# Kernel optimization log

Hardware: AMD Instinct MI355X
Metric: run time of the kernel (lower is better)

The kernel has to match this reference:

```python
import jax, jax.numpy as jnp
import numpy as np

DIM_MODEL = 1024
HEADS = 16
DIM_PER_HEAD = DIM_MODEL // HEADS


def setup_inputs() -> dict:
    key = jax.random.key(0)
    k0, k1, k2, k3, k4 = jax.random.split(key, 5)
    x = jax.random.normal(k0, (2, 2048, DIM_MODEL), dtype=jnp.float32)
    # combined_linear: dim_model -> 3*dim_model (torch Linear: y = x @ W.T + b)
    s_in = 1.0 / np.sqrt(DIM_MODEL)
    W_qkv = jax.random.uniform(k1, (3 * DIM_MODEL, DIM_MODEL), minval=-s_in, maxval=s_in, dtype=jnp.float32)
    b_qkv = jax.random.uniform(k2, (3 * DIM_MODEL,), minval=-s_in, maxval=s_in, dtype=jnp.float32)
    W_out = jax.random.uniform(k3, (DIM_MODEL, DIM_MODEL), minval=-s_in, maxval=s_in, dtype=jnp.float32)
    b_out = jax.random.uniform(k4, (DIM_MODEL,), minval=-s_in, maxval=s_in, dtype=jnp.float32)
    return {"x": x, "W_qkv": W_qkv, "b_qkv": b_qkv, "W_out": W_out, "b_out": b_out}


def reference(x, W_qkv, b_qkv, W_out, b_out):
    B, S, D = x.shape
    H, Dh = HEADS, DIM_PER_HEAD
    qkv = x @ W_qkv.T + b_qkv  # [B, S, 3D]
    q, k, v = jnp.split(qkv, 3, axis=2)
    # [B, H, S, Dh]
    q = q.reshape(B, S, H, Dh).transpose(0, 2, 1, 3)
    k = k.reshape(B, S, H, Dh).transpose(0, 2, 1, 3)
    v = v.reshape(B, S, H, Dh).transpose(0, 2, 1, 3)
    scores = jnp.einsum('bhqd,bhkd->bhqk', q, k) / jnp.sqrt(jnp.float32(Dh))
    causal = jnp.tril(jnp.ones((S, S), dtype=bool))
    scores = jnp.where(causal[None, None, :, :], scores, -jnp.inf)
    p_attn = jax.nn.softmax(scores, axis=-1)
    out = jnp.einsum('bhqk,bhkd->bhqd', p_attn, v)
    out = out.transpose(0, 2, 1, 3).reshape(B, S, D)
    return out @ W_out.T + b_out
```

## Files before the change

kernel.cpp:

```cpp
#include <hip/hip_runtime.h>
#include <cstdint>

typedef __attribute__((ext_vector_type(8))) __bf16 bf16x8;
typedef __attribute__((ext_vector_type(4))) float f32x4;
typedef __attribute__((ext_vector_type(8))) short short8;
typedef __attribute__((ext_vector_type(4))) float float4v;
typedef __attribute__((ext_vector_type(4))) unsigned uint4v;
typedef __attribute__((ext_vector_type(4))) unsigned short ushort4v;

__device__ __forceinline__ unsigned short f2bf(float f) {
    unsigned u = __builtin_bit_cast(unsigned, f);
    u += 0x7fffu + ((u >> 16) & 1u);
    return (unsigned short)(u >> 16);
}
__device__ __forceinline__ float bf2f(unsigned short s) {
    return __builtin_bit_cast(float, (unsigned)s << 16);
}
__device__ __forceinline__ f32x4 mfma_bf16(bf16x8 a, bf16x8 b, f32x4 c) {
    return __builtin_amdgcn_mfma_f32_16x16x32_bf16(a, b, c, 0, 0, 0);
}
__device__ __forceinline__ unsigned pkbf(float lo, float hi) {
    unsigned r;
    asm("v_cvt_pk_bf16_f32 %0, %1, %2" : "=v"(r) : "v"(lo), "v"(hi));
    return r;
}

#define GLD16(g, l)                                                                     \
    __builtin_amdgcn_global_load_lds((const __attribute__((address_space(1))) void*)(g), \
                                     (__attribute__((address_space(3))) void*)(l), 16, 0, 0)

__global__ void __launch_bounds__(256) cvt_all(const float* __restrict__ x,
                                               const float* __restrict__ wqkv,
                                               const float* __restrict__ wout,
                                               unsigned short* __restrict__ xb,
                                               unsigned short* __restrict__ wqb,
                                               unsigned short* __restrict__ wob) {
    int i = blockIdx.x * blockDim.x + threadIdx.x;
#pragma unroll
    for (int k = 0; k < 2; k++, i += 524288) {
        const float* s;
        unsigned short* d;
        int off;
        if (i < 524288)      { s = x;    d = xb;  off = i; }
        else if (i < 917504) { s = wqkv; d = wqb; off = i - 524288; }
        else                 { s = wout; d = wob; off = i - 917504; }
        const float4v* sp = (const float4v*)(s + (size_t)off * 8);
        float4v v0 = sp[0], v1 = sp[1];
        uint4v u;
        u[0] = pkbf(v0[0], v0[1]);
        u[1] = pkbf(v0[2], v0[3]);
        u[2] = pkbf(v1[0], v1[1]);
        u[3] = pkbf(v1[2], v1[3]);
        *(uint4v*)(d + (size_t)off * 8) = u;
    }
}

template <int MODE>
__global__ void __launch_bounds__(256) gemm_bt(const unsigned short* __restrict__ A,
                                               const unsigned short* __restrict__ B,
                                               const float* __restrict__ bias,
                                               void* __restrict__ C,
                                               unsigned short* __restrict__ vT,
                                               int M, int N, int K) {
    __shared__ __attribute__((aligned(16))) unsigned short As[2][128 * 32];
    __shared__ __attribute__((aligned(16))) unsigned short Bs[2][128 * 32];
    const int tid = threadIdx.x;
    const int w = tid >> 6, lane = tid & 63;
    const int a = lane & 15, g = lane >> 4;

    const int cpx = gridDim.x >> 3;
    const int nf = ((int)blockIdx.x & 7) * cpx + ((int)blockIdx.x >> 3);
    const int bx = nf >> 5;
    const int by = nf & 31;
    const int m0 = by * 128, n0 = bx * 128;
    const int wr = (w >> 1) * 64, wc = (w & 1) * 64;

    f32x4 acc[4][4];
#pragma unroll
    for (int i = 0; i < 4; i++)
#pragma unroll
        for (int j = 0; j < 4; j++) acc[i][j] = (f32x4)(0.0f);

    const int r0 = tid >> 2;
    const int c0 = (tid & 3) * 8;
    const unsigned short* gA0 = A + (size_t)(m0 + r0) * K + c0;
    const unsigned short* gA1 = A + (size_t)(m0 + 64 + r0) * K + c0;
    const unsigned short* gB0 = B + (size_t)(n0 + r0) * K + c0;
    const unsigned short* gB1 = B + (size_t)(n0 + 64 + r0) * K + c0;

#define GSTAGE(buf_, k0_)                                               \
    {                                                                   \
        char* la_ = (char*)&As[buf_][0] + w * 1024;                     \
        char* lb_ = (char*)&Bs[buf_][0] + w * 1024;                     \
        GLD16(gA0 + (k0_), la_);                                        \
        GLD16(gA1 + (k0_), la_ + 4096);                                 \
        GLD16(gB0 + (k0_), lb_);                                        \
        GLD16(gB1 + (k0_), lb_ + 4096);                                 \
    }

    GSTAGE(0, 0);
    __syncthreads();

    int cur = 0;
    for (int k0 = 0; k0 < K; k0 += 32) {
        if (k0 + 32 < K) GSTAGE(cur ^ 1, k0 + 32);

        bf16x8 af[4], bfr[4];
#pragma unroll
        for (int i = 0; i < 4; i++) {
            af[i]  = *(const bf16x8*)&As[cur][(wr + i * 16 + a) * 32 + g * 8];
            bfr[i] = *(const bf16x8*)&Bs[cur][(wc + i * 16 + a) * 32 + g * 8];
        }
#pragma unroll
        for (int i = 0; i < 4; i++)
#pragma unroll
            for (int j = 0; j < 4; j++) acc[i][j] = mfma_bf16(af[i], bfr[j], acc[i][j]);

        __syncthreads();
        cur ^= 1;
    }
#undef GSTAGE

#pragma unroll
    for (int j = 0; j < 4; j++) {
        const int col = n0 + wc + j * 16 + a;
        const float bv = bias[col];
        if (MODE == 0) {
            float* Cf = (float*)C;
#pragma unroll
            for (int i = 0; i < 4; i++)
#pragma unroll
                for (int jr = 0; jr < 4; jr++) {
                    const int row = m0 + wr + i * 16 + g * 4 + jr;
                    Cf[(size_t)row * N + col] = acc[i][j][jr] + bv;
                }
        } else if (n0 < 2048) {
            unsigned short* Cb = (unsigned short*)C;
#pragma unroll
            for (int i = 0; i < 4; i++)
#pragma unroll
                for (int jr = 0; jr < 4; jr++) {
                    const int row = m0 + wr + i * 16 + g * 4 + jr;
                    Cb[(size_t)row * 2048 + col] = f2bf(acc[i][j][jr] + bv);
                }
        } else {
            const int vd = col - 2048;
            const int hh = vd >> 6, dd = vd & 63;
#pragma unroll
            for (int i = 0; i < 4; i++) {
                const int token0 = m0 + wr + i * 16 + g * 4;
                const int bb = token0 >> 11, kl = token0 & 2047;
                ushort4v st;
#pragma unroll
                for (int jr = 0; jr < 4; jr++) st[jr] = f2bf(acc[i][j][jr] + bv);
                *(ushort4v*)(vT + ((size_t)((bb << 4) + hh) * 64 + dd) * 2048 + kl) = st;
            }
        }
    }
}


#define STAGE(bf_, t_)                                                  \
    {                                                                   \
        const size_t ko_ = (size_t)(t_) * 128 * LDQ;                    \
        const size_t vo_ = (size_t)(t_) * 128;                          \
        char* db_ = (char*)&KV[bf_][0] + w * 1024;                      \
        GLD16(sK0 + ko_, db_);                                          \
        GLD16(sK1 + ko_, db_ + 8192);                                   \
        GLD16(sV0 + vo_, db_ + 16384);                                  \
        GLD16(sV1 + vo_, db_ + 24576);                                  \
    }

__global__ void __launch_bounds__(512, 4) attn_fwd(const unsigned short* __restrict__ qk,
                                                   const unsigned short* __restrict__ vT,
                                                   unsigned short* __restrict__ o) {
    constexpr int SL = 2048, DH = 64, LDQ = 2048;
    constexpr float GAMMA = 0.18033688011112042f;
    const int bh = blockIdx.x & 31;
    const int s = blockIdx.x >> 5;
    const int qb = (s < 8) ? 15 - s : s - 8;
    const int b = bh >> 4, h = bh & 15;
    const int tid = threadIdx.x;
    const int w = tid >> 6, lane = tid & 63;
    const int n = lane & 15, g = lane >> 4;

    __shared__ __attribute__((aligned(16))) unsigned short KV[2][16384];

    const int qs = qb * 128 + w * 16 + n;
    const int nt = qb + 1;

    bf16x8 qf[2];
    {
        const unsigned short* qp = qk + (size_t)(b * SL + qs) * LDQ + h * DH + g * 8;
        short8 la = *(const short8*)qp, lb = *(const short8*)(qp + 32);
        short8 s0, s1;
#pragma unroll
        for (int e = 0; e < 8; e++) {
            s0[e] = (short)f2bf(bf2f((unsigned short)la[e]) * GAMMA);
            s1[e] = (short)f2bf(bf2f((unsigned short)lb[e]) * GAMMA);
        }
        qf[0] = __builtin_bit_cast(bf16x8, s0);
        qf[1] = __builtin_bit_cast(bf16x8, s1);
    }

    const int rK = tid >> 3;
    const int xrK = (rK & 3) | (((rK >> 3) & 1) << 2);
    const int csK = (((tid & 7) ^ xrK) << 3);
    const unsigned short* sK0 = qk + (size_t)(b * SL + rK) * LDQ + 1024 + h * DH + csK;
    const unsigned short* sK1 = sK0 + (size_t)64 * LDQ;
    const int dV = tid >> 4;
    const int csV = (((tid & 15) ^ (dV & 7)) << 3);
    const unsigned short* sV0 = vT + (size_t)bh * DH * SL + (size_t)dV * SL + csV;
    const unsigned short* sV1 = sV0 + (size_t)32 * SL;

    const int srow = 8 * (n >> 2) + (n & 3);
    const int xrq = (n & 3) | (((n >> 2) & 1) << 2);
    const int offK0 = ((g ^ xrq) << 3);
    const int offK1 = offK0 ^ 32;
    int offV[4];
#pragma unroll
    for (int kc = 0; kc < 4; kc++) offV[kc] = (((4 * kc + g) ^ (n & 7)) << 3);

    f32x4 of[4];
#pragma unroll
    for (int i = 0; i < 4; i++) of[i] = (f32x4)(0.0f);
    float m_i = -1e30f, l_i = 0.0f;

    STAGE(0, 0);
    __syncthreads();

    for (int t = 0; t < nt; ++t) {
        const unsigned short* kvb = &KV[t & 1][0];
        if (t + 1 < nt) STAGE((t & 1) ^ 1, t + 1);

        f32x4 p[8];
        __builtin_amdgcn_s_setprio(1);
#pragma unroll
        for (int f = 0; f < 8; f++) {
            const int r_ = srow + ((f >> 1) << 5) + ((f & 1) << 2);
            const bf16x8 ka_ = *(const bf16x8*)&kvb[r_ * 64 + offK0];
            const bf16x8 kc_ = *(const bf16x8*)&kvb[r_ * 64 + offK1];
            f32x4 acc_ = (f32x4)(0.0f);
            acc_ = mfma_bf16(ka_, qf[0], acc_);
            acc_ = mfma_bf16(kc_, qf[1], acc_);
            p[f] = acc_;
        }
        __builtin_amdgcn_s_setprio(0);

        if (t == nt - 1) {
            const int k0 = t * 128;
#pragma unroll
            for (int f = 0; f < 8; f++) {
                const int kb_ = k0 + ((f >> 1) << 5) + ((f & 1) << 2) + 8 * g;
#pragma unroll
                for (int e = 0; e < 4; e++)
                    if (kb_ + e > qs) p[f][e] = -1e30f;
            }
        }

        float mx = -1e30f;
#pragma unroll
        for (int f = 0; f < 8; f++) {
            const float a_ = fmaxf(fmaxf(p[f][0], p[f][1]), fmaxf(p[f][2], p[f][3]));
            mx = fmaxf(mx, a_);
        }
        mx = fmaxf(mx, __shfl_xor(mx, 16));
        mx = fmaxf(mx, __shfl_xor(mx, 32));
        if (!__all(mx <= m_i + 8.0f)) {
            const float mn_ = fmaxf(m_i, mx);
            const float al_ = __builtin_amdgcn_exp2f(m_i - mn_);
            l_i *= al_;
#pragma unroll
            for (int d_ = 0; d_ < 4; d_++) of[d_] = of[d_] * al_;
            m_i = mn_;
        }
        float rs = 0.0f;
#pragma unroll
        for (int f = 0; f < 8; f++)
#pragma unroll
            for (int e = 0; e < 4; e++) {
                p[f][e] = __builtin_amdgcn_exp2f(p[f][e] - m_i);
                rs += p[f][e];
            }
        l_i += rs;

        bf16x8 pf[4];
#pragma unroll
        for (int kc = 0; kc < 4; kc++) {
            uint4v u_;
            u_[0] = pkbf(p[2 * kc][0], p[2 * kc][1]);
            u_[1] = pkbf(p[2 * kc][2], p[2 * kc][3]);
            u_[2] = pkbf(p[2 * kc + 1][0], p[2 * kc + 1][1]);
            u_[3] = pkbf(p[2 * kc + 1][2], p[2 * kc + 1][3]);
            pf[kc] = __builtin_bit_cast(bf16x8, u_);
        }

        const unsigned short* vb = kvb + 8192;
        __builtin_amdgcn_s_setprio(1);
#pragma unroll
        for (int df = 0; df < 4; df++) {
            const int vrow = (df * 16 + n) * 128;
#pragma unroll
            for (int kc = 0; kc < 4; kc++) {
                const bf16x8 va_ = *(const bf16x8*)&vb[vrow + offV[kc]];
                of[df] = mfma_bf16(va_, pf[kc], of[df]);
            }
        }
        __builtin_amdgcn_s_setprio(0);

        __syncthreads();
    }

    float rl = l_i;
    rl += __shfl_xor(rl, 16);
    rl += __shfl_xor(rl, 32);
    const float inv = 1.0f / rl;
    unsigned short* op = o + (size_t)(b * SL + qs) * 1024 + h * DH + 4 * g;
#pragma unroll
    for (int df = 0; df < 4; df++) {
        ushort4v st;
#pragma unroll
        for (int r = 0; r < 4; r++) st[r] = f2bf(of[df][r] * inv);
        *(ushort4v*)(op + df * 16) = st;
    }
}

extern "C" void kernel_launch(void* const* d_in, const int* in_sizes, int n_in,
                              void* d_out, int out_size, void* d_ws, size_t ws_size,
                              hipStream_t stream) {
    (void)in_sizes; (void)n_in; (void)out_size; (void)ws_size;
    const float* x    = (const float*)d_in[0];
    const float* Wqkv = (const float*)d_in[1];
    const float* bqkv = (const float*)d_in[2];
    const float* Wout = (const float*)d_in[3];
    const float* bout = (const float*)d_in[4];
    float* out = (float*)d_out;

    const int BS = 2, SL = 2048, DM = 1024;
    const int M = BS * SL;
    const int N1 = 3 * DM;
    const int K = DM;

    char* ws = (char*)d_ws;
    unsigned short* x_bf    = (unsigned short*)(ws);
    unsigned short* wqkv_bf = (unsigned short*)(ws + (8u << 20));
    unsigned short* wout_bf = (unsigned short*)(ws + (14u << 20));
    unsigned short* qkbuf   = (unsigned short*)(ws + (16u << 20));
    unsigned short* vTbuf   = (unsigned short*)(ws + (32u << 20));
    unsigned short* attn_o  = (unsigned short*)(ws + (40u << 20));

    cvt_all<<<2048, 256, 0, stream>>>(x, Wqkv, Wout, x_bf, wqkv_bf, wout_bf);

    gemm_bt<1><<<dim3(N1 / 128 * (M / 128)), 256, 0, stream>>>(x_bf, wqkv_bf, bqkv, qkbuf, vTbuf, M, N1, K);

    attn_fwd<<<dim3(512), 512, 0, stream>>>(qkbuf, vTbuf, attn_o);

    gemm_bt<0><<<dim3(DM / 128 * (M / 128)), 256, 0, stream>>>(attn_o, wout_bf, bout, out, nullptr, M, DM, K);
}
```

Baseline: 105.1 us.

## Add dedicated 256x192-tile QKV GEMM with swizzled LDS and interleaved staging

```diff
diff --git a/kernel.cpp b/kernel.cpp
--- a/kernel.cpp
+++ b/kernel.cpp
@@ -55,12 +55,126 @@
     }
 }
 
-template <int MODE>
+
+#define STG_A(bf_, i_, t_) \
+    GLD16(gA + (size_t)(i_) * 64 * 1024 + (size_t)(t_) * 64, (char*)&Asl[bf_][0] + (i_) * 8192 + w * 1024)
+#define STG_B(bf_, i_, t_) \
+    GLD16(gB + (size_t)(i_) * 64 * 1024 + (size_t)(t_) * 64, (char*)&Bsl[bf_][0] + (i_) * 8192 + w * 1024)
+
+#define LDA(c_, mf_, kk_) \
+    (*(const bf16x8*)((const char*)&Asl[c_][0] + (wm * 128 + (mf_) * 16 + a) * 128 + (((((kk_) << 2) + g) ^ xa) << 4)))
+#define LDB(c_, nf_, kk_) \
+    (*(const bf16x8*)((const char*)&Bsl[c_][0] + (wn * 48 + (nf_) * 16 + a) * 128 + (((((kk_) << 2) + g) ^ xa) << 4)))
+
+#define PHASE(c_, mb_)                                                        \
+    {                                                                         \
+        bf16x8 a0_ = LDA(c_, mb_, 0), a1_ = LDA(c_, mb_, 1);                  \
+        bf16x8 a2_ = LDA(c_, (mb_) + 1, 0), a3_ = LDA(c_, (mb_) + 1, 1);      \
+        __builtin_amdgcn_s_setprio(1);                                        \
+        _Pragma("unroll") for (int nf_ = 0; nf_ < 3; nf_++) {                 \
+            acc[mb_][nf_]       = mfma_bf16(a0_, bfr[nf_][0], acc[mb_][nf_]);       \
+            acc[mb_][nf_]       = mfma_bf16(a1_, bfr[nf_][1], acc[mb_][nf_]);       \
+            acc[(mb_) + 1][nf_] = mfma_bf16(a2_, bfr[nf_][0], acc[(mb_) + 1][nf_]); \
+            acc[(mb_) + 1][nf_] = mfma_bf16(a3_, bfr[nf_][1], acc[(mb_) + 1][nf_]); \
+        }                                                                     \
+        __builtin_amdgcn_s_setprio(0);                                        \
+    }
+
+__global__ void __launch_bounds__(512, 2) gemm_qkv(const unsigned short* __restrict__ A,
+                                                   const unsigned short* __restrict__ B,
+                                                   const float* __restrict__ bias,
+                                                   unsigned short* __restrict__ qkbuf,
+                                                   unsigned short* __restrict__ vT) {
+    constexpr int K = 1024;
+    __shared__ __attribute__((aligned(16))) unsigned short Asl[2][256 * 64];
+    __shared__ __attribute__((aligned(16))) unsigned short Bsl[2][192 * 64];
+    const int tid = threadIdx.x;
+    const int w = tid >> 6, lane = tid & 63;
+    const int a = lane & 15, g = lane >> 4;
+    const int xa = a & 7;
+    const int wm = w >> 2, wn = w & 3;
+
+    const int nfb = ((int)blockIdx.x & 7) * 32 + ((int)blockIdx.x >> 3);
+    const int bx = nfb >> 4, by = nfb & 15;
+    const int m0 = by * 256, n0 = bx * 192;
+
+    f32x4 acc[8][3];
+#pragma unroll
+    for (int i = 0; i < 8; i++)
+#pragma unroll
+        for (int j = 0; j < 3; j++) acc[i][j] = (f32x4)(0.0f);
+
+    const int rA = tid >> 3, uA = tid & 7;
+    const unsigned short* gA = A + (size_t)(m0 + rA) * K + ((uA ^ (rA & 7)) << 3);
+    const unsigned short* gB = B + (size_t)(n0 + rA) * K + ((uA ^ (rA & 7)) << 3);
+
+    STG_A(0, 0, 0); STG_A(0, 1, 0); STG_A(0, 2, 0); STG_A(0, 3, 0);
+    STG_B(0, 0, 0); STG_B(0, 1, 0); STG_B(0, 2, 0);
+
+    for (int t = 0; t < 16; ++t) {
+        const int c = t & 1, nx = c ^ 1;
+        const bool more = (t < 15);
+
+        if (more) { STG_A(nx, 0, t + 1); STG_A(nx, 1, t + 1); }
+        if (more) asm volatile("s_waitcnt vmcnt(2)" ::: "memory");
+        else      asm volatile("s_waitcnt vmcnt(0)" ::: "memory");
+        __builtin_amdgcn_s_barrier();
+
+        bf16x8 bfr[3][2];
+#pragma unroll
+        for (int nf = 0; nf < 3; nf++) {
+            bfr[nf][0] = LDB(c, nf, 0);
+            bfr[nf][1] = LDB(c, nf, 1);
+        }
+        PHASE(c, 0);
+        __builtin_amdgcn_s_barrier();
+
+        if (more) { STG_A(nx, 2, t + 1); STG_A(nx, 3, t + 1); }
+        PHASE(c, 2);
+        __builtin_amdgcn_s_barrier();
+
+        if (more) { STG_B(nx, 0, t + 1); STG_B(nx, 1, t + 1); }
+        PHASE(c, 4);
+        __builtin_amdgcn_s_barrier();
+
+        if (more) { STG_B(nx, 2, t + 1); }
+        PHASE(c, 6);
+        asm volatile("" ::: "memory");
+        __builtin_amdgcn_s_barrier();
+    }
+
+#pragma unroll
+    for (int nf = 0; nf < 3; nf++) {
+        const int cb = n0 + wn * 48 + nf * 16;
+        const int col = cb + a;
+        const float bv = bias[col];
+        if (cb < 2048) {
+#pragma unroll
+            for (int mf = 0; mf < 8; mf++)
+#pragma unroll
+                for (int jr = 0; jr < 4; jr++) {
+                    const int row = m0 + wm * 128 + mf * 16 + g * 4 + jr;
+                    qkbuf[(size_t)row * 2048 + col] = f2bf(acc[mf][nf][jr] + bv);
+                }
+        } else {
+            const int vd = col - 2048, hh = vd >> 6, dd = vd & 63;
+#pragma unroll
+            for (int mf = 0; mf < 8; mf++) {
+                const int t0 = m0 + wm * 128 + mf * 16 + g * 4;
+                const int bb = t0 >> 11, kl = t0 & 2047;
+                ushort4v st;
+#pragma unroll
+                for (int jr = 0; jr < 4; jr++) st[jr] = f2bf(acc[mf][nf][jr] + bv);
+                *(ushort4v*)(vT + ((size_t)((bb << 4) + hh) * 64 + dd) * 2048 + kl) = st;
+            }
+        }
+    }
+}
+
 __global__ void __launch_bounds__(256) gemm_bt(const unsigned short* __restrict__ A,
                                                const unsigned short* __restrict__ B,
                                                const float* __restrict__ bias,
-                                               void* __restrict__ C,
-                                               unsigned short* __restrict__ vT,
+                                               float* __restrict__ C,
                                                int M, int N, int K) {
     __shared__ __attribute__((aligned(16))) unsigned short As[2][128 * 32];
     __shared__ __attribute__((aligned(16))) unsigned short Bs[2][128 * 32];
@@ -125,37 +239,13 @@
     for (int j = 0; j < 4; j++) {
         const int col = n0 + wc + j * 16 + a;
         const float bv = bias[col];
-        if (MODE == 0) {
-            float* Cf = (float*)C;
-#pragma unroll
-            for (int i = 0; i < 4; i++)
-#pragma unroll
-                for (int jr = 0; jr < 4; jr++) {
-                    const int row = m0 + wr + i * 16 + g * 4 + jr;
-                    Cf[(size_t)row * N + col] = acc[i][j][jr] + bv;
-                }
-        } else if (n0 < 2048) {
-            unsigned short* Cb = (unsigned short*)C;
-#pragma unroll
-            for (int i = 0; i < 4; i++)
-#pragma unroll
-                for (int jr = 0; jr < 4; jr++) {
-                    const int row = m0 + wr + i * 16 + g * 4 + jr;
-                    Cb[(size_t)row * 2048 + col] = f2bf(acc[i][j][jr] + bv);
-                }
-        } else {
-            const int vd = col - 2048;
-            const int hh = vd >> 6, dd = vd & 63;
-#pragma unroll
-            for (int i = 0; i < 4; i++) {
-                const int token0 = m0 + wr + i * 16 + g * 4;
-                const int bb = token0 >> 11, kl = token0 & 2047;
-                ushort4v st;
-#pragma unroll
-                for (int jr = 0; jr < 4; jr++) st[jr] = f2bf(acc[i][j][jr] + bv);
-                *(ushort4v*)(vT + ((size_t)((bb << 4) + hh) * 64 + dd) * 2048 + kl) = st;
+#pragma unroll
+        for (int i = 0; i < 4; i++)
+#pragma unroll
+            for (int jr = 0; jr < 4; jr++) {
+                const int row = m0 + wr + i * 16 + g * 4 + jr;
+                C[(size_t)row * N + col] = acc[i][j][jr] + bv;
             }
-        }
     }
 }
 
@@ -338,7 +428,6 @@
 
     const int BS = 2, SL = 2048, DM = 1024;
     const int M = BS * SL;
-    const int N1 = 3 * DM;
     const int K = DM;
 
     char* ws = (char*)d_ws;
@@ -351,9 +440,9 @@
 
     cvt_all<<<2048, 256, 0, stream>>>(x, Wqkv, Wout, x_bf, wqkv_bf, wout_bf);
 
-    gemm_bt<1><<<dim3(N1 / 128 * (M / 128)), 256, 0, stream>>>(x_bf, wqkv_bf, bqkv, qkbuf, vTbuf, M, N1, K);
+    gemm_qkv<<<dim3(256), 512, 0, stream>>>(x_bf, wqkv_bf, bqkv, qkbuf, vTbuf);
 
     attn_fwd<<<dim3(512), 512, 0, stream>>>(qkbuf, vTbuf, attn_o);
 
-    gemm_bt<0><<<dim3(DM / 128 * (M / 128)), 256, 0, stream>>>(attn_o, wout_bf, bout, out, nullptr, M, DM, K);
-}
+    gemm_bt<<<dim3(256), 256, 0, stream>>>(attn_o, wout_bf, bout, out, M, DM, K);
+}
```

Measured after the change: 115.4 us. 1.1x slower.
